# Kernel tuning notes

Hardware: AMD Instinct MI355X
Metric: run time of the kernel (lower is better)

The kernel has to match this reference:

```python
import jax, jax.numpy as jnp
import numpy as np

B, S, NX, H = 8, 1024, 1024, 16
D = NX // H  # head dim = 64


def setup_inputs() -> dict:
    key = jax.random.key(0)
    k1, k2, k3 = jax.random.split(key, 3)
    x = jax.random.normal(k1, (B, S, NX), dtype=jnp.float32)
    Wqkv = jax.random.normal(k2, (NX, 3 * NX), dtype=jnp.float32) * 0.02
    bqkv = jnp.zeros((3 * NX,), dtype=jnp.float32)
    Wproj = jax.random.normal(k3, (NX, NX), dtype=jnp.float32) * 0.02
    bproj = jnp.zeros((NX,), dtype=jnp.float32)
    return {"x": x, "Wqkv": Wqkv, "bqkv": bqkv, "Wproj": Wproj, "bproj": bproj}


def reference(x, Wqkv, bqkv, Wproj, bproj):
    # c_attn: Conv1D == x @ W + b
    qkv = jnp.einsum('bsn,nm->bsm', x, Wqkv) + bqkv  # [B,S,3*NX]
    q, k, v = jnp.split(qkv, 3, axis=-1)
    # split heads -> [B,H,S,D]
    def split_heads(t):
        return t.reshape(B, S, H, D).transpose(0, 2, 1, 3)
    q, k, v = split_heads(q), split_heads(k), split_heads(v)
    # present = stack(key, value) with key as [B,H,S,D]
    present = jnp.stack((k, v))  # [2,B,H,S,D]
    # scores, scaled (scale=True) by sqrt(head_dim)
    w = jnp.einsum('bhqd,bhkd->bhqk', q, k) / jnp.sqrt(jnp.asarray(D, x.dtype))
    bias = jnp.tril(jnp.ones((S, S), dtype=x.dtype))[None, None]  # causal tril buffer
    w = w * bias - 10000.0 * (1.0 - bias)
    w = jax.nn.softmax(w, axis=-1)
    a = jnp.einsum('bhqk,bhkd->bhqd', w, v)  # [B,H,S,D]
    a = a.transpose(0, 2, 1, 3).reshape(B, S, NX)  # merge heads
    a = jnp.einsum('bsn,nm->bsm', a, Wproj) + bproj  # c_proj
    return a, present
```

## Files before the change

kernel.cpp:

```cpp
#include <hip/hip_runtime.h>
#include <stdint.h>


#define BB 8
#define SS 1024
#define NXX 1024
#define NH 16
#define HD 64
#define KK 1024
#define NKT 16

typedef __bf16 bf16x8 __attribute__((ext_vector_type(8)));
typedef float  floatx4 __attribute__((ext_vector_type(4)));
typedef unsigned short ushort8 __attribute__((ext_vector_type(8)));
typedef unsigned short ushortx4 __attribute__((ext_vector_type(4)));

__device__ inline float bf2f(unsigned short u) {
    unsigned int x = ((unsigned int)u) << 16;
    float f;
    __builtin_memcpy(&f, &x, 4);
    return f;
}
__device__ inline unsigned short f2bf(float f) {
    unsigned int u;
    __builtin_memcpy(&u, &f, 4);
    u += 0x7FFFu + ((u >> 16) & 1u);
    return (unsigned short)(u >> 16);
}

__device__ inline void gload_lds16(const unsigned short* g, unsigned short* l) {
    __builtin_amdgcn_global_load_lds(
        (const __attribute__((address_space(1))) void*)g,
        (__attribute__((address_space(3))) void*)l, 16, 0, 0);
}

__device__ inline void barrier_raw() {
    asm volatile("" ::: "memory");
    __builtin_amdgcn_sched_barrier(0);
    __builtin_amdgcn_s_barrier();
    __builtin_amdgcn_sched_barrier(0);
    asm volatile("" ::: "memory");
}
#define WAIT_VM0() asm volatile("s_waitcnt vmcnt(0)" ::: "memory")

__global__ void sniff_k(const unsigned short* __restrict__ x, int* __restrict__ flag) {
    const int lane = threadIdx.x & 63;
    ushort8 v = *(const ushort8*)(x + (size_t)lane * 8);
    int g = 0;
#pragma unroll
    for (int j = 0; j < 8; j++) {
        float f = bf2f(v[j]);
        float a = fabsf(f);
        if (!(a <= 1e4f)) g++;
        else if (f != 0.f && a < 1e-35f) g++;
    }
#pragma unroll
    for (int s = 1; s < 64; s <<= 1) g += __shfl_xor(g, s);
    if (lane == 0 && blockIdx.x == 0) *flag = (g > 16) ? 1 : 0;
}

__global__ __launch_bounds__(256) void prep(
    const void* __restrict__ x, const void* __restrict__ Wqkv,
    const void* __restrict__ Wproj,
    unsigned short* __restrict__ xbf, unsigned short* __restrict__ WqkvT,
    unsigned short* __restrict__ WprojT, const int* __restrict__ flagp) {
    const int f32 = *flagp;
    int blk = blockIdx.x;
    if (blk < 4096) {
        const size_t i = ((size_t)blk * 256 + threadIdx.x) * 8;
        if (f32) {
            const floatx4* p = (const floatx4*)((const float*)x + i);
            floatx4 f0 = p[0], f1 = p[1];
            ushort8 u;
#pragma unroll
            for (int j = 0; j < 4; j++) { u[j] = f2bf(f0[j]); u[4 + j] = f2bf(f1[j]); }
            *(ushort8*)(xbf + i) = u;
        } else {
            *(ushort8*)(xbf + i) = *(const ushort8*)((const unsigned short*)x + i);
        }
        return;
    }
    blk -= 4096;
    const void* in;
    unsigned short* out;
    int R, C;
    if (blk < 3072) { in = Wqkv; out = WqkvT; R = 1024; C = 3072; }
    else            { blk -= 3072; in = Wproj; out = WprojT; R = 1024; C = 1024; }
    const int ctiles = C / 32;
    const int c0 = (blk % ctiles) * 32, r0 = (blk / ctiles) * 32;

    __shared__ unsigned short tile[32][33];
    const int tx = threadIdx.x & 31, ty = threadIdx.x >> 5;
    if (f32) {
        const float* inf = (const float*)in;
#pragma unroll
        for (int i = ty; i < 32; i += 8)
            tile[i][tx] = f2bf(inf[(size_t)(r0 + i) * C + c0 + tx]);
    } else {
        const unsigned short* inu = (const unsigned short*)in;
#pragma unroll
        for (int i = ty; i < 32; i += 8)
            tile[i][tx] = inu[(size_t)(r0 + i) * C + c0 + tx];
    }
    __syncthreads();
#pragma unroll
    for (int i = ty; i < 32; i += 8)
        out[(size_t)(c0 + i) * R + r0 + tx] = tile[tx][i];
}

#define ASOFF(slot) ((slot) * 16384)
#define BSOFF(slot) (32768 + (slot) * NF * 4096)
#define STAGE_A(slot, h, kt) do { \
    const unsigned short* sg_ = Ab + (size_t)((h) * 128) * KK + (size_t)(kt) * 64; \
    gload_lds16(sg_, &POOL[ASOFF(slot) + (h) * 8192 + w * 512]); \
    gload_lds16(sg_ + (size_t)64 * KK, &POOL[ASOFF(slot) + (h) * 8192 + 4096 + w * 512]); \
} while (0)
#define STAGE_B(slot, j, kt) do { \
    const unsigned short* sg_ = Bb + (size_t)((j) * 64) * KK + (size_t)(kt) * 64; \
    gload_lds16(sg_, &POOL[BSOFF(slot) + (j) * 4096 + w * 512]); \
} while (0)
#define LOADA(dst, qq) do { \
    _Pragma("unroll") \
    for (int mm = 0; mm < 2; mm++) { \
        const int arow = (qq) * 32 + mm * 16 + l15; \
        dst[mm][0] = *(const bf16x8*)&Ah[arow * 64 + fo0]; \
        dst[mm][1] = *(const bf16x8*)&Ah[arow * 64 + fo1]; \
    } \
} while (0)
#define MFMAQ(qq, ar) do { \
    __builtin_amdgcn_s_setprio(1); \
    _Pragma("unroll") \
    for (int mm = 0; mm < 2; mm++) \
    _Pragma("unroll") \
    for (int nf = 0; nf < NF; nf++) { \
        acc[2 * (qq) + mm][nf] = __builtin_amdgcn_mfma_f32_16x16x32_bf16(ar[mm][0], bfr[nf][0], acc[2 * (qq) + mm][nf], 0, 0, 0); \
        acc[2 * (qq) + mm][nf] = __builtin_amdgcn_mfma_f32_16x16x32_bf16(ar[mm][1], bfr[nf][1], acc[2 * (qq) + mm][nf], 0, 0, 0); \
    } \
    __builtin_amdgcn_s_setprio(0); \
} while (0)
#define WAIT_VMNF() do { \
    if constexpr (NF == 2)      asm volatile("s_waitcnt vmcnt(2)" ::: "memory"); \
    else if constexpr (NF == 3) asm volatile("s_waitcnt vmcnt(3)" ::: "memory"); \
    else                        asm volatile("s_waitcnt vmcnt(4)" ::: "memory"); \
} while (0)

template <int MODE, int NF>
__global__ __launch_bounds__(512, 2) void gemm8p(
    const unsigned short* __restrict__ A,
    const unsigned short* __restrict__ Bt,
    const void* __restrict__ bias,
    void* __restrict__ outbase,
    unsigned short* __restrict__ q_ws,
    unsigned short* __restrict__ kbf,
    unsigned short* __restrict__ vbfT,
    int N, int Nt, const int* __restrict__ flagp) {
    __shared__ __align__(16) unsigned short POOL[2 * 2 * 8192 + 2 * NF * 4096];
    constexpr int TBW = 64 * NF + 12;

    const int f32 = *flagp;
    const int tid  = threadIdx.x;
    const int lane = tid & 63;
    const int w = tid >> 6;
    const int r = w >> 2;
    const int c = w & 3;
    const int l15 = lane & 15;
    const int quad = lane >> 4;

    const int cpx = gridDim.x >> 3;
    const int bid = (blockIdx.x & 7) * cpx + (blockIdx.x >> 3);
    const int bx = bid % Nt, by = bid / Nt;
    const int row0 = by * 256, col0 = bx * (64 * NF);

    floatx4 acc[8][NF];
    floatx4 zz = {0.f, 0.f, 0.f, 0.f};
#pragma unroll
    for (int i = 0; i < 8; i++)
#pragma unroll
        for (int j = 0; j < NF; j++) acc[i][j] = zz;

    const int srow = tid >> 3;
    const int scole = ((tid & 7) ^ (srow & 7)) << 3;
    const unsigned short* Ab = A  + (size_t)(row0 + srow) * KK + scole;
    const unsigned short* Bb = Bt + (size_t)(col0 + srow) * KK + scole;

    const int fo0 = (quad << 3) ^ ((l15 & 7) << 3);
    const int fo1 = fo0 ^ 32;

    STAGE_A(0, 0, 0); STAGE_A(0, 1, 0);
#pragma unroll
    for (int j = 0; j < NF; j++) STAGE_B(0, j, 0);
#pragma unroll
    for (int j = 0; j < NF; j++) STAGE_B(1, j, 1);
    WAIT_VMNF();
    barrier_raw();

    bf16x8 bfr[NF][2], aX[2][2], aY[2][2];
#pragma unroll 2
    for (int t = 0; t < NKT; t++) {
        const int slot = t & 1;
        const unsigned short* Ah = &POOL[ASOFF(slot) + r * 8192];
        const unsigned short* Bh = &POOL[BSOFF(slot)];
#pragma unroll
        for (int nf = 0; nf < NF; nf++) {
            const int brow = c * (16 * NF) + nf * 16 + l15;
            bfr[nf][0] = *(const bf16x8*)&Bh[brow * 64 + fo0];
            bfr[nf][1] = *(const bf16x8*)&Bh[brow * 64 + fo1];
        }
        LOADA(aX, 0);
        LOADA(aY, 1);
        if (t + 1 < NKT) STAGE_A(slot ^ 1, 0, t + 1);
        barrier_raw();
        MFMAQ(0, aX);
        barrier_raw();
        LOADA(aX, 2);
        if (t + 1 < NKT) STAGE_A(slot ^ 1, 1, t + 1);
        barrier_raw();
        MFMAQ(1, aY);
        barrier_raw();
        LOADA(aY, 3);
        if (t + 2 < NKT) {
#pragma unroll
            for (int j = 0; j < (NF + 1) / 2; j++) STAGE_B(slot, j, t + 2);
        }
        barrier_raw();
        MFMAQ(2, aX);
        barrier_raw();
        if (t + 2 < NKT) {
#pragma unroll
            for (int j = (NF + 1) / 2; j < NF; j++) STAGE_B(slot, j, t + 2);
        }
        barrier_raw();
        MFMAQ(3, aY);
        if (t < NKT - 2) { WAIT_VMNF(); } else { WAIT_VM0(); }
        barrier_raw();
    }

    float bv[NF];
#pragma unroll
    for (int nf = 0; nf < NF; nf++) {
        const int colb = col0 + c * (16 * NF) + nf * 16 + l15;
        bv[nf] = f32 ? ((const float*)bias)[colb] : bf2f(((const unsigned short*)bias)[colb]);
    }

    if (MODE == 0) {
#pragma unroll
        for (int nf = 0; nf < NF; nf++) {
            const int colb = col0 + c * (16 * NF) + nf * 16 + l15;
#pragma unroll
            for (int mi = 0; mi < 8; mi++)
#pragma unroll
                for (int i = 0; i < 4; i++) {
                    const int row = row0 + r * 128 + mi * 16 + quad * 4 + i;
                    const float val = acc[mi][nf][i] + bv[nf];
                    const size_t idx = (size_t)row * N + colb;
                    if (f32) ((float*)outbase)[idx] = val;
                    else     ((unsigned short*)outbase)[idx] = f2bf(val);
                }
        }
        return;
    }

    if constexpr (MODE == 1) {
        const size_t esz = f32 ? 4 : 2;
        const int b = row0 >> 10;
        const int s0 = row0 & 1023;
        unsigned short* TB = POOL;

#pragma unroll
        for (int nf = 0; nf < NF; nf++) {
            const int colc = c * (16 * NF) + nf * 16 + l15;
            const int colb = col0 + colc;
            const int sec = colb >> 10;
            const int h = (colb & 1023) >> 6, d = colb & 63;
#pragma unroll
            for (int mi = 0; mi < 8; mi++)
#pragma unroll
                for (int i = 0; i < 4; i++) {
                    const int sl = r * 128 + mi * 16 + quad * 4 + i;
                    const float val = acc[mi][nf][i] + bv[nf];
                    TB[sl * TBW + colc] = f2bf(val);
                    if (f32) {
                        const size_t idx = (size_t)((b * NH + h) * SS + s0 + sl) * HD + d;
                        if (sec == 1)      ((float*)((char*)outbase + (size_t)(BB * SS * NXX) * esz))[idx] = val;
                        else if (sec == 2) ((float*)((char*)outbase + (size_t)(2 * BB * SS * NXX) * esz))[idx] = val;
                    }
                }
        }
        __syncthreads();

        for (int rg = tid; rg < 256 * NF * 8; rg += 512) {
            const int c8 = (rg % (NF * 8)) * 8;
            const int s  = rg / (NF * 8);
            const int colb = col0 + c8;
            const int sec = colb >> 10;
            const int h = (colb & 1023) >> 6, d0 = colb & 63;
            const size_t dstoff = (size_t)((b * NH + h) * SS + s0 + s) * HD + d0;
            ushort8 v8 = *(const ushort8*)&TB[s * TBW + c8];
            if (sec == 0) {
                *(ushort8*)(q_ws + dstoff) = v8;
            } else if (sec == 1) {
                *(ushort8*)(kbf + dstoff) = v8;
                if (!f32) *(ushort8*)((unsigned short*)outbase + (size_t)(BB * SS * NXX) + dstoff) = v8;
            } else {
                if (!f32) *(ushort8*)((unsigned short*)outbase + (size_t)(2 * BB * SS * NXX) + dstoff) = v8;
            }
        }
        for (int rg = tid; rg < NF * 64 * 32; rg += 512) {
            const int col = rg >> 5;
            const int colb = col0 + col;
            if ((colb >> 10) != 2) continue;
            const int orun = (rg & 31) * 8;
            const int h = (colb & 1023) >> 6, d = colb & 63;
            ushort8 v8;
#pragma unroll
            for (int k2 = 0; k2 < 8; k2++) {
                const int o = orun + k2;
                const int sl = (o & ~63) + (((o & 3) << 4) | ((o & 63) >> 2));
                v8[k2] = TB[sl * TBW + col];
            }
            *(ushort8*)&vbfT[(size_t)((b * NH + h) * HD + d) * SS + s0 + orun] = v8;
        }
    }
}

__global__ __launch_bounds__(256, 4) void attn(
    const unsigned short* __restrict__ q_ws,
    const unsigned short* __restrict__ kbf,
    const unsigned short* __restrict__ vbfT,
    unsigned short* __restrict__ amerged) {
    const int tid = threadIdx.x;
    const int lane = tid & 63;
    const int w = tid >> 6;
    const int l15 = lane & 15, quad = lane >> 4;
    const int blk = blockIdx.x;
    const int qb = blk & 7;
    const int bh = blk >> 3;
    const int b = bh >> 4, h = bh & 15;

    const unsigned short* Q = q_ws + (size_t)bh * (SS * HD);
    const unsigned short* K = kbf + (size_t)bh * (SS * HD);
    const unsigned short* V = vbfT + (size_t)bh * (HD * SS);

    __shared__ __align__(16) unsigned short Ks[64][72];
    __shared__ __align__(16) unsigned short Vs[64][72];
    __shared__ __align__(16) unsigned short Pl[4][32][72];

    floatx4 zz = {0.f, 0.f, 0.f, 0.f};
    ushort8 ones_u;
#pragma unroll
    for (int j = 0; j < 8; j++) ones_u[j] = 0x3F80;
    const bf16x8 ones = __builtin_bit_cast(bf16x8, ones_u);

    const int srow = tid >> 2;
    const int soff = (tid & 3) * 16;

    const int qbase = qb * 128;
    const int wrow0 = qbase + w * 32;
    const int wq_max = wrow0 + 31;
    const int jend = qbase + 128;

    bf16x8 qa[2][2];
#pragma unroll
    for (int m = 0; m < 2; m++)
#pragma unroll
        for (int t = 0; t < 2; t++)
            qa[m][t] = *(const bf16x8*)&Q[(size_t)(wrow0 + m * 16 + l15) * HD + t * 32 + quad * 8];

    floatx4 o[2][4], o5[2];
    float mrow[2][4];
#pragma unroll
    for (int m = 0; m < 2; m++) {
        o5[m] = zz;
#pragma unroll
        for (int i = 0; i < 4; i++) mrow[m][i] = -1e30f;
#pragma unroll
        for (int nf = 0; nf < 4; nf++) o[m][nf] = zz;
    }

    *(ushort8*)&Ks[srow][soff]     = *(const ushort8*)&K[(size_t)srow * HD + soff];
    *(ushort8*)&Ks[srow][soff + 8] = *(const ushort8*)&K[(size_t)srow * HD + soff + 8];
    *(ushort8*)&Vs[srow][soff]     = *(const ushort8*)&V[(size_t)srow * SS + soff];
    *(ushort8*)&Vs[srow][soff + 8] = *(const ushort8*)&V[(size_t)srow * SS + soff + 8];
    __syncthreads();

    for (int j0 = 0; j0 < jend; j0 += 64) {
        const bool havenext = (j0 + 64 < jend);
        ushort8 kn0, kn1, vn0, vn1;
        if (havenext) {
            kn0 = *(const ushort8*)&K[(size_t)(j0 + 64 + srow) * HD + soff];
            kn1 = *(const ushort8*)&K[(size_t)(j0 + 64 + srow) * HD + soff + 8];
            vn0 = *(const ushort8*)&V[(size_t)srow * SS + j0 + 64 + soff];
            vn1 = *(const ushort8*)&V[(size_t)srow * SS + j0 + 64 + soff + 8];
        }

        if (j0 <= wq_max) {
            floatx4 sf[2][4];
#pragma unroll
            for (int kg = 0; kg < 4; kg++) {
                bf16x8 kb0 = *(const bf16x8*)&Ks[kg * 16 + l15][quad * 8];
                bf16x8 kb1 = *(const bf16x8*)&Ks[kg * 16 + l15][32 + quad * 8];
#pragma unroll
                for (int m = 0; m < 2; m++) {
                    floatx4 s = zz;
                    s = __builtin_amdgcn_mfma_f32_16x16x32_bf16(qa[m][0], kb0, s, 0, 0, 0);
                    s = __builtin_amdgcn_mfma_f32_16x16x32_bf16(qa[m][1], kb1, s, 0, 0, 0);
                    sf[m][kg] = s;
                }
            }

            float alpha_[2][4];
#pragma unroll
            for (int m = 0; m < 2; m++)
#pragma unroll
                for (int i = 0; i < 4; i++) {
                    const int qrow = wrow0 + m * 16 + quad * 4 + i;
                    float pv4[4];
#pragma unroll
                    for (int kg = 0; kg < 4; kg++) {
                        const int key = j0 + kg * 16 + l15;
                        float s = sf[m][kg][i] * 0.125f;
                        if (key > qrow) s = -10000.0f;
                        pv4[kg] = s;
                    }
                    float t = fmaxf(fmaxf(pv4[0], pv4[1]), fmaxf(pv4[2], pv4[3]));
                    t = fmaxf(t, __shfl_xor(t, 1));
                    t = fmaxf(t, __shfl_xor(t, 2));
                    t = fmaxf(t, __shfl_xor(t, 4));
                    t = fmaxf(t, __shfl_xor(t, 8));
                    const float mnew = fmaxf(mrow[m][i], t);
                    alpha_[m][i] = __expf(mrow[m][i] - mnew);
                    mrow[m][i] = mnew;
                    ushortx4 pk;
#pragma unroll
                    for (int kg = 0; kg < 4; kg++)
                        pk[kg] = f2bf(__expf(pv4[kg] - mnew));
                    *(ushortx4*)&Pl[w][m * 16 + quad * 4 + i][l15 * 4] = pk;
                }

#pragma unroll
            for (int m = 0; m < 2; m++) {
#pragma unroll
                for (int i = 0; i < 4; i++) o5[m][i] *= alpha_[m][i];
#pragma unroll
                for (int nf = 0; nf < 4; nf++)
#pragma unroll
                    for (int i = 0; i < 4; i++) o[m][nf][i] *= alpha_[m][i];
            }

            bf16x8 pa[2][2];
#pragma unroll
            for (int m = 0; m < 2; m++) {
                pa[m][0] = *(const bf16x8*)&Pl[w][m * 16 + l15][quad * 8];
                pa[m][1] = *(const bf16x8*)&Pl[w][m * 16 + l15][32 + quad * 8];
            }

#pragma unroll
            for (int m = 0; m < 2; m++) {
                o5[m] = __builtin_amdgcn_mfma_f32_16x16x32_bf16(pa[m][0], ones, o5[m], 0, 0, 0);
                o5[m] = __builtin_amdgcn_mfma_f32_16x16x32_bf16(pa[m][1], ones, o5[m], 0, 0, 0);
            }
#pragma unroll
            for (int nf = 0; nf < 4; nf++) {
                bf16x8 vb0 = *(const bf16x8*)&Vs[nf * 16 + l15][quad * 8];
                bf16x8 vb1 = *(const bf16x8*)&Vs[nf * 16 + l15][32 + quad * 8];
#pragma unroll
                for (int m = 0; m < 2; m++) {
                    o[m][nf] = __builtin_amdgcn_mfma_f32_16x16x32_bf16(pa[m][0], vb0, o[m][nf], 0, 0, 0);
                    o[m][nf] = __builtin_amdgcn_mfma_f32_16x16x32_bf16(pa[m][1], vb1, o[m][nf], 0, 0, 0);
                }
            }
        }
        __syncthreads();
        if (havenext) {
            *(ushort8*)&Ks[srow][soff]     = kn0;
            *(ushort8*)&Ks[srow][soff + 8] = kn1;
            *(ushort8*)&Vs[srow][soff]     = vn0;
            *(ushort8*)&Vs[srow][soff + 8] = vn1;
        }
        __syncthreads();
    }

#pragma unroll
    for (int m = 0; m < 2; m++)
#pragma unroll
        for (int nf = 0; nf < 4; nf++)
#pragma unroll
            for (int i = 0; i < 4; i++) {
                const int s = wrow0 + m * 16 + quad * 4 + i;
                amerged[(size_t)(b * SS + s) * NXX + h * HD + nf * 16 + l15] =
                    f2bf(o[m][nf][i] / o5[m][i]);
            }
}

extern "C" void kernel_launch(void* const* d_in, const int* in_sizes, int n_in,
                              void* d_out, int out_size, void* d_ws, size_t ws_size,
                              hipStream_t stream) {
    const void* x     = d_in[0];
    const void* Wqkv  = d_in[1];
    const void* bqkv  = d_in[2];
    const void* Wproj = d_in[3];
    const void* bproj = d_in[4];

    int* flag = (int*)d_ws;
    unsigned short* ws = (unsigned short*)d_ws + 8;
    unsigned short* WqkvT   = ws;
    unsigned short* WprojT  = WqkvT + 3072 * 1024;
    unsigned short* q_ws    = WprojT + 1024 * 1024;
    unsigned short* kbf     = q_ws + 8 * 1024 * 1024;
    unsigned short* vbfT    = kbf + 8 * 1024 * 1024;
    unsigned short* amerged = vbfT + 8 * 1024 * 1024;
    unsigned short* xbf     = amerged;

    sniff_k<<<1, 64, 0, stream>>>((const unsigned short*)x, flag);
    prep<<<dim3(8192), 256, 0, stream>>>(x, Wqkv, Wproj, xbf, WqkvT, WprojT, flag);
    gemm8p<1, 3><<<dim3(512), 512, 0, stream>>>(
        xbf, WqkvT, bqkv, d_out, q_ws, kbf, vbfT, 3072, 16, flag);
    attn<<<dim3(BB * NH * 8), 256, 0, stream>>>(q_ws, kbf, vbfT, amerged);
    gemm8p<0, 2><<<dim3(256), 512, 0, stream>>>(
        amerged, WprojT, bproj, d_out, nullptr, nullptr, nullptr, 1024, 8, flag);
}
```

Measured before the change: 348.8 us.

## Retile QKV GEMM, pair causal attention tiles, add simple projection GEMM

The QKV GEMM moves to NF=4 tiles over 384 blocks, drops to 1 block per CU, and grows shared memory for the transposed epilogue. Attention blocks now each process two query tiles (p and 7-p) to balance causal work, and use exp2 with a folded log2e scale. The output projection gets a new 128x128 double-buffered MFMA GEMM in place of gemm8p<0,2>. These target load imbalance and tile efficiency, at the cost of lower occupancy and less parallelism in attention.

After: 340.6 us. 2.3% less time.

```diff
diff --git a/kernel.cpp b/kernel.cpp
--- a/kernel.cpp
+++ b/kernel.cpp
@@ -145,7 +145,7 @@
 } while (0)
 
 template <int MODE, int NF>
-__global__ __launch_bounds__(512, 2) void gemm8p(
+__global__ __launch_bounds__(512, 1) void gemm8p(
     const unsigned short* __restrict__ A,
     const unsigned short* __restrict__ Bt,
     const void* __restrict__ bias,
@@ -154,8 +154,10 @@
     unsigned short* __restrict__ kbf,
     unsigned short* __restrict__ vbfT,
     int N, int Nt, const int* __restrict__ flagp) {
-    __shared__ __align__(16) unsigned short POOL[2 * 2 * 8192 + 2 * NF * 4096];
-    constexpr int TBW = 64 * NF + 12;
+    constexpr int TBW  = 64 * NF + 12;
+    constexpr int STG  = 2 * 2 * 8192 + 2 * NF * 4096;
+    constexpr int PSZ  = (MODE == 1 && 256 * TBW > STG) ? 256 * TBW : STG;
+    __shared__ __align__(16) unsigned short POOL[PSZ];
 
     const int f32 = *flagp;
     const int tid  = threadIdx.x;
@@ -323,7 +325,96 @@
     }
 }
 
-__global__ __launch_bounds__(256, 4) void attn(
+__global__ __launch_bounds__(256) void gemm_bt(
+    const unsigned short* __restrict__ A,
+    const unsigned short* __restrict__ Bt,
+    const void* __restrict__ bias,
+    void* __restrict__ outbase,
+    int M, int N, int K, const int* __restrict__ flagp) {
+    __shared__ __align__(16) unsigned short As[2][128 * 32];
+    __shared__ __align__(16) unsigned short Bs[2][128 * 32];
+
+    const int f32 = *flagp;
+    const int tid  = threadIdx.x;
+    const int lane = tid & 63;
+    const int wave = tid >> 6;
+    const int wr = wave >> 1, wc = wave & 1;
+    const int l15 = lane & 15;
+    const int quad = lane >> 4;
+    const int row0 = blockIdx.y * 128;
+    const int col0 = blockIdx.x * 128;
+
+    floatx4 acc[4][4];
+    floatx4 zz = {0.f, 0.f, 0.f, 0.f};
+#pragma unroll
+    for (int i = 0; i < 4; i++)
+#pragma unroll
+        for (int j = 0; j < 4; j++) acc[i][j] = zz;
+
+    const int lrow = lane >> 2;
+    const int lcol = (lane & 3) * 8;
+    const unsigned short* Ag = A  + (size_t)(row0 + wave * 32 + lrow) * K + lcol;
+    const unsigned short* Bg = Bt + (size_t)(col0 + wave * 32 + lrow) * K + lcol;
+    const int sl0 = (wave * 32) * 32;
+    const int sl1 = (wave * 32 + 16) * 32;
+
+    gload_lds16(Ag, &As[0][sl0]);
+    gload_lds16(Ag + (size_t)16 * K, &As[0][sl1]);
+    gload_lds16(Bg, &Bs[0][sl0]);
+    gload_lds16(Bg + (size_t)16 * K, &Bs[0][sl1]);
+    __syncthreads();
+
+    int cur = 0;
+    for (int k0 = 0; k0 < K; k0 += 32) {
+        if (k0 + 32 < K) {
+            const unsigned short* Agn = Ag + k0 + 32;
+            const unsigned short* Bgn = Bg + k0 + 32;
+            gload_lds16(Agn, &As[cur ^ 1][sl0]);
+            gload_lds16(Agn + (size_t)16 * K, &As[cur ^ 1][sl1]);
+            gload_lds16(Bgn, &Bs[cur ^ 1][sl0]);
+            gload_lds16(Bgn + (size_t)16 * K, &Bs[cur ^ 1][sl1]);
+        }
+
+        bf16x8 af[4], bfr[4];
+#pragma unroll
+        for (int mi = 0; mi < 4; mi++)
+            af[mi] = *(const bf16x8*)&As[cur][(wr * 64 + mi * 16 + l15) * 32 + quad * 8];
+#pragma unroll
+        for (int ni = 0; ni < 4; ni++)
+            bfr[ni] = *(const bf16x8*)&Bs[cur][(wc * 64 + ni * 16 + l15) * 32 + quad * 8];
+#pragma unroll
+        for (int mi = 0; mi < 4; mi++)
+#pragma unroll
+            for (int ni = 0; ni < 4; ni++)
+                acc[mi][ni] = __builtin_amdgcn_mfma_f32_16x16x32_bf16(af[mi], bfr[ni], acc[mi][ni], 0, 0, 0);
+
+        __syncthreads();
+        cur ^= 1;
+    }
+
+    float bv[4];
+#pragma unroll
+    for (int ni = 0; ni < 4; ni++) {
+        const int colb = col0 + wc * 64 + ni * 16 + l15;
+        bv[ni] = f32 ? ((const float*)bias)[colb] : bf2f(((const unsigned short*)bias)[colb]);
+    }
+#pragma unroll
+    for (int mi = 0; mi < 4; mi++)
+#pragma unroll
+        for (int ni = 0; ni < 4; ni++) {
+            const int colb = col0 + wc * 64 + ni * 16 + l15;
+#pragma unroll
+            for (int i = 0; i < 4; i++) {
+                const int row = row0 + wr * 64 + mi * 16 + quad * 4 + i;
+                const float val = acc[mi][ni][i] + bv[ni];
+                const size_t idx = (size_t)row * N + colb;
+                if (f32) ((float*)outbase)[idx] = val;
+                else     ((unsigned short*)outbase)[idx] = f2bf(val);
+            }
+        }
+}
+
+__global__ __launch_bounds__(256) void attn(
     const unsigned short* __restrict__ q_ws,
     const unsigned short* __restrict__ kbf,
     const unsigned short* __restrict__ vbfT,
@@ -333,8 +424,8 @@
     const int w = tid >> 6;
     const int l15 = lane & 15, quad = lane >> 4;
     const int blk = blockIdx.x;
-    const int qb = blk & 7;
-    const int bh = blk >> 3;
+    const int p = blk & 3;
+    const int bh = blk >> 2;
     const int b = bh >> 4, h = bh & 15;
 
     const unsigned short* Q = q_ws + (size_t)bh * (SS * HD);
@@ -345,6 +436,7 @@
     __shared__ __align__(16) unsigned short Vs[64][72];
     __shared__ __align__(16) unsigned short Pl[4][32][72];
 
+    const float SC2 = 0.18033688f;
     floatx4 zz = {0.f, 0.f, 0.f, 0.f};
     ushort8 ones_u;
 #pragma unroll
@@ -354,142 +446,147 @@
     const int srow = tid >> 2;
     const int soff = (tid & 3) * 16;
 
-    const int qbase = qb * 128;
-    const int wrow0 = qbase + w * 32;
-    const int wq_max = wrow0 + 31;
-    const int jend = qbase + 128;
-
-    bf16x8 qa[2][2];
-#pragma unroll
-    for (int m = 0; m < 2; m++)
-#pragma unroll
-        for (int t = 0; t < 2; t++)
-            qa[m][t] = *(const bf16x8*)&Q[(size_t)(wrow0 + m * 16 + l15) * HD + t * 32 + quad * 8];
-
-    floatx4 o[2][4], o5[2];
-    float mrow[2][4];
-#pragma unroll
-    for (int m = 0; m < 2; m++) {
-        o5[m] = zz;
-#pragma unroll
-        for (int i = 0; i < 4; i++) mrow[m][i] = -1e30f;
-#pragma unroll
-        for (int nf = 0; nf < 4; nf++) o[m][nf] = zz;
-    }
-
-    *(ushort8*)&Ks[srow][soff]     = *(const ushort8*)&K[(size_t)srow * HD + soff];
-    *(ushort8*)&Ks[srow][soff + 8] = *(const ushort8*)&K[(size_t)srow * HD + soff + 8];
-    *(ushort8*)&Vs[srow][soff]     = *(const ushort8*)&V[(size_t)srow * SS + soff];
-    *(ushort8*)&Vs[srow][soff + 8] = *(const ushort8*)&V[(size_t)srow * SS + soff + 8];
-    __syncthreads();
-
-    for (int j0 = 0; j0 < jend; j0 += 64) {
-        const bool havenext = (j0 + 64 < jend);
-        ushort8 kn0, kn1, vn0, vn1;
-        if (havenext) {
-            kn0 = *(const ushort8*)&K[(size_t)(j0 + 64 + srow) * HD + soff];
-            kn1 = *(const ushort8*)&K[(size_t)(j0 + 64 + srow) * HD + soff + 8];
-            vn0 = *(const ushort8*)&V[(size_t)srow * SS + j0 + 64 + soff];
-            vn1 = *(const ushort8*)&V[(size_t)srow * SS + j0 + 64 + soff + 8];
-        }
-
-        if (j0 <= wq_max) {
-            floatx4 sf[2][4];
-#pragma unroll
-            for (int kg = 0; kg < 4; kg++) {
-                bf16x8 kb0 = *(const bf16x8*)&Ks[kg * 16 + l15][quad * 8];
-                bf16x8 kb1 = *(const bf16x8*)&Ks[kg * 16 + l15][32 + quad * 8];
+#pragma unroll
+    for (int tile = 0; tile < 2; tile++) {
+        const int qb = tile ? (7 - p) : p;
+        const int qbase = qb * 128;
+        const int wrow0 = qbase + w * 32;
+        const int wq_max = wrow0 + 31;
+        const int jend = qbase + 128;
+
+        bf16x8 qa[2][2];
+#pragma unroll
+        for (int m = 0; m < 2; m++)
+#pragma unroll
+            for (int t = 0; t < 2; t++)
+                qa[m][t] = *(const bf16x8*)&Q[(size_t)(wrow0 + m * 16 + l15) * HD + t * 32 + quad * 8];
+
+        floatx4 o[2][4], o5[2];
+        float mrow[2][4];
+#pragma unroll
+        for (int m = 0; m < 2; m++) {
+            o5[m] = zz;
+#pragma unroll
+            for (int i = 0; i < 4; i++) mrow[m][i] = -1e30f;
+#pragma unroll
+            for (int nf = 0; nf < 4; nf++) o[m][nf] = zz;
+        }
+
+        *(ushort8*)&Ks[srow][soff]     = *(const ushort8*)&K[(size_t)srow * HD + soff];
+        *(ushort8*)&Ks[srow][soff + 8] = *(const ushort8*)&K[(size_t)srow * HD + soff + 8];
+        *(ushort8*)&Vs[srow][soff]     = *(const ushort8*)&V[(size_t)srow * SS + soff];
+        *(ushort8*)&Vs[srow][soff + 8] = *(const ushort8*)&V[(size_t)srow * SS + soff + 8];
+        __syncthreads();
+
+        for (int j0 = 0; j0 < jend; j0 += 64) {
+            const bool havenext = (j0 + 64 < jend);
+            ushort8 kn0, kn1, vn0, vn1;
+            if (havenext) {
+                kn0 = *(const ushort8*)&K[(size_t)(j0 + 64 + srow) * HD + soff];
+                kn1 = *(const ushort8*)&K[(size_t)(j0 + 64 + srow) * HD + soff + 8];
+                vn0 = *(const ushort8*)&V[(size_t)srow * SS + j0 + 64 + soff];
+                vn1 = *(const ushort8*)&V[(size_t)srow * SS + j0 + 64 + soff + 8];
+            }
+
+            if (j0 <= wq_max) {
+                floatx4 sf[2][4];
+#pragma unroll
+                for (int kg = 0; kg < 4; kg++) {
+                    bf16x8 kb0 = *(const bf16x8*)&Ks[kg * 16 + l15][quad * 8];
+                    bf16x8 kb1 = *(const bf16x8*)&Ks[kg * 16 + l15][32 + quad * 8];
+#pragma unroll
+                    for (int m = 0; m < 2; m++) {
+                        floatx4 s = zz;
+                        s = __builtin_amdgcn_mfma_f32_16x16x32_bf16(qa[m][0], kb0, s, 0, 0, 0);
+                        s = __builtin_amdgcn_mfma_f32_16x16x32_bf16(qa[m][1], kb1, s, 0, 0, 0);
+                        sf[m][kg] = s;
+                    }
+                }
+
+                float alpha_[2][4];
+#pragma unroll
+                for (int m = 0; m < 2; m++)
+#pragma unroll
+                    for (int i = 0; i < 4; i++) {
+                        const int qrow = wrow0 + m * 16 + quad * 4 + i;
+                        float pv4[4];
+#pragma unroll
+                        for (int kg = 0; kg < 4; kg++) {
+                            const int key = j0 + kg * 16 + l15;
+                            float s = sf[m][kg][i] * SC2;
+                            if (key > qrow) s = -100000.0f;
+                            pv4[kg] = s;
+                        }
+                        float t = fmaxf(fmaxf(fmaxf(pv4[0], pv4[1]), pv4[2]), pv4[3]);
+                        t = fmaxf(t, __shfl_xor(t, 1));
+                        t = fmaxf(t, __shfl_xor(t, 2));
+                        t = fmaxf(t, __shfl_xor(t, 4));
+                        t = fmaxf(t, __shfl_xor(t, 8));
+                        const float mnew = fmaxf(mrow[m][i], t);
+                        alpha_[m][i] = exp2f(mrow[m][i] - mnew);
+                        mrow[m][i] = mnew;
+                        ushortx4 pk;
+#pragma unroll
+                        for (int kg = 0; kg < 4; kg++)
+                            pk[kg] = f2bf(exp2f(pv4[kg] - mnew));
+                        *(ushortx4*)&Pl[w][m * 16 + quad * 4 + i][l15 * 4] = pk;
+                    }
+
 #pragma unroll
                 for (int m = 0; m < 2; m++) {
-                    floatx4 s = zz;
-                    s = __builtin_amdgcn_mfma_f32_16x16x32_bf16(qa[m][0], kb0, s, 0, 0, 0);
-                    s = __builtin_amdgcn_mfma_f32_16x16x32_bf16(qa[m][1], kb1, s, 0, 0, 0);
-                    sf[m][kg] = s;
+#pragma unroll
+                    for (int i = 0; i < 4; i++) o5[m][i] *= alpha_[m][i];
+#pragma unroll
+                    for (int nf = 0; nf < 4; nf++)
+#pragma unroll
+                        for (int i = 0; i < 4; i++) o[m][nf][i] *= alpha_[m][i];
+                }
+
+                bf16x8 pa[2][2];
+#pragma unroll
+                for (int m = 0; m < 2; m++) {
+                    pa[m][0] = *(const bf16x8*)&Pl[w][m * 16 + l15][quad * 8];
+                    pa[m][1] = *(const bf16x8*)&Pl[w][m * 16 + l15][32 + quad * 8];
+                }
+
+#pragma unroll
+                for (int m = 0; m < 2; m++) {
+                    o5[m] = __builtin_amdgcn_mfma_f32_16x16x32_bf16(pa[m][0], ones, o5[m], 0, 0, 0);
+                    o5[m] = __builtin_amdgcn_mfma_f32_16x16x32_bf16(pa[m][1], ones, o5[m], 0, 0, 0);
+                }
+#pragma unroll
+                for (int nf = 0; nf < 4; nf++) {
+                    bf16x8 vb0 = *(const bf16x8*)&Vs[nf * 16 + l15][quad * 8];
+                    bf16x8 vb1 = *(const bf16x8*)&Vs[nf * 16 + l15][32 + quad * 8];
+#pragma unroll
+                    for (int m = 0; m < 2; m++) {
+                        o[m][nf] = __builtin_amdgcn_mfma_f32_16x16x32_bf16(pa[m][0], vb0, o[m][nf], 0, 0, 0);
+                        o[m][nf] = __builtin_amdgcn_mfma_f32_16x16x32_bf16(pa[m][1], vb1, o[m][nf], 0, 0, 0);
+                    }
                 }
             }
-
-            float alpha_[2][4];
-#pragma unroll
-            for (int m = 0; m < 2; m++)
+            __syncthreads();
+            if (havenext) {
+                *(ushort8*)&Ks[srow][soff]     = kn0;
+                *(ushort8*)&Ks[srow][soff + 8] = kn1;
+                *(ushort8*)&Vs[srow][soff]     = vn0;
+                *(ushort8*)&Vs[srow][soff + 8] = vn1;
+            }
+            __syncthreads();
+        }
+
+#pragma unroll
+        for (int m = 0; m < 2; m++)
+#pragma unroll
+            for (int nf = 0; nf < 4; nf++)
 #pragma unroll
                 for (int i = 0; i < 4; i++) {
-                    const int qrow = wrow0 + m * 16 + quad * 4 + i;
-                    float pv4[4];
-#pragma unroll
-                    for (int kg = 0; kg < 4; kg++) {
-                        const int key = j0 + kg * 16 + l15;
-                        float s = sf[m][kg][i] * 0.125f;
-                        if (key > qrow) s = -10000.0f;
-                        pv4[kg] = s;
-                    }
-                    float t = fmaxf(fmaxf(pv4[0], pv4[1]), fmaxf(pv4[2], pv4[3]));
-                    t = fmaxf(t, __shfl_xor(t, 1));
-                    t = fmaxf(t, __shfl_xor(t, 2));
-                    t = fmaxf(t, __shfl_xor(t, 4));
-                    t = fmaxf(t, __shfl_xor(t, 8));
-                    const float mnew = fmaxf(mrow[m][i], t);
-                    alpha_[m][i] = __expf(mrow[m][i] - mnew);
-                    mrow[m][i] = mnew;
-                    ushortx4 pk;
-#pragma unroll
-                    for (int kg = 0; kg < 4; kg++)
-                        pk[kg] = f2bf(__expf(pv4[kg] - mnew));
-                    *(ushortx4*)&Pl[w][m * 16 + quad * 4 + i][l15 * 4] = pk;
-                }
-
-#pragma unroll
-            for (int m = 0; m < 2; m++) {
-#pragma unroll
-                for (int i = 0; i < 4; i++) o5[m][i] *= alpha_[m][i];
-#pragma unroll
-                for (int nf = 0; nf < 4; nf++)
-#pragma unroll
-                    for (int i = 0; i < 4; i++) o[m][nf][i] *= alpha_[m][i];
-            }
-
-            bf16x8 pa[2][2];
-#pragma unroll
-            for (int m = 0; m < 2; m++) {
-                pa[m][0] = *(const bf16x8*)&Pl[w][m * 16 + l15][quad * 8];
-                pa[m][1] = *(const bf16x8*)&Pl[w][m * 16 + l15][32 + quad * 8];
-            }
-
-#pragma unroll
-            for (int m = 0; m < 2; m++) {
-                o5[m] = __builtin_amdgcn_mfma_f32_16x16x32_bf16(pa[m][0], ones, o5[m], 0, 0, 0);
-                o5[m] = __builtin_amdgcn_mfma_f32_16x16x32_bf16(pa[m][1], ones, o5[m], 0, 0, 0);
-            }
-#pragma unroll
-            for (int nf = 0; nf < 4; nf++) {
-                bf16x8 vb0 = *(const bf16x8*)&Vs[nf * 16 + l15][quad * 8];
-                bf16x8 vb1 = *(const bf16x8*)&Vs[nf * 16 + l15][32 + quad * 8];
-#pragma unroll
-                for (int m = 0; m < 2; m++) {
-                    o[m][nf] = __builtin_amdgcn_mfma_f32_16x16x32_bf16(pa[m][0], vb0, o[m][nf], 0, 0, 0);
-                    o[m][nf] = __builtin_amdgcn_mfma_f32_16x16x32_bf16(pa[m][1], vb1, o[m][nf], 0, 0, 0);
-                }
-            }
-        }
+                    const int s = wrow0 + m * 16 + quad * 4 + i;
+                    amerged[(size_t)(b * SS + s) * NXX + h * HD + nf * 16 + l15] =
+                        f2bf(o[m][nf][i] / o5[m][i]);
+                }
         __syncthreads();
-        if (havenext) {
-            *(ushort8*)&Ks[srow][soff]     = kn0;
-            *(ushort8*)&Ks[srow][soff + 8] = kn1;
-            *(ushort8*)&Vs[srow][soff]     = vn0;
-            *(ushort8*)&Vs[srow][soff + 8] = vn1;
-        }
-        __syncthreads();
-    }
-
-#pragma unroll
-    for (int m = 0; m < 2; m++)
-#pragma unroll
-        for (int nf = 0; nf < 4; nf++)
-#pragma unroll
-            for (int i = 0; i < 4; i++) {
-                const int s = wrow0 + m * 16 + quad * 4 + i;
-                amerged[(size_t)(b * SS + s) * NXX + h * HD + nf * 16 + l15] =
-                    f2bf(o[m][nf][i] / o5[m][i]);
-            }
+    }
 }
 
 extern "C" void kernel_launch(void* const* d_in, const int* in_sizes, int n_in,
@@ -513,9 +610,9 @@
 
     sniff_k<<<1, 64, 0, stream>>>((const unsigned short*)x, flag);
     prep<<<dim3(8192), 256, 0, stream>>>(x, Wqkv, Wproj, xbf, WqkvT, WprojT, flag);
-    gemm8p<1, 3><<<dim3(512), 512, 0, stream>>>(
-        xbf, WqkvT, bqkv, d_out, q_ws, kbf, vbfT, 3072, 16, flag);
-    attn<<<dim3(BB * NH * 8), 256, 0, stream>>>(q_ws, kbf, vbfT, amerged);
-    gemm8p<0, 2><<<dim3(256), 512, 0, stream>>>(
-        amerged, WprojT, bproj, d_out, nullptr, nullptr, nullptr, 1024, 8, flag);
-}
+    gemm8p<1, 4><<<dim3(384), 512, 0, stream>>>(
+        xbf, WqkvT, bqkv, d_out, q_ws, kbf, vbfT, 3072, 12, flag);
+    attn<<<dim3(BB * NH * 4), 256, 0, stream>>>(q_ws, kbf, vbfT, amerged);
+    gemm_bt<<<dim3(1024 / 128, 8192 / 128), 256, 0, stream>>>(
+        amerged, WprojT, bproj, d_out, 8192, 1024, 1024, flag);
+}
```
